# Kernel tuning notes

Hardware: AMD Instinct MI355X
Metric: run time of the kernel (lower is better)

## Reference

```python
import jax, jax.numpy as jnp
import numpy as np
from jax import lax

B, H0, W0 = 4, 64, 64
IN_DIM = 256; DIM = 256; HEADS = 8; WS = 8; HID = 1024
DH = DIM // HEADS          # 32, per-head dim
P = 16; K = 16             # DES decomposition: 256 = K * P


def hardswish(x):
    return x * jnp.clip(x + 3.0, 0.0, 6.0) * (1.0 / 6.0)


def layernorm(x, w, b):
    mu = jnp.mean(x, -1, keepdims=True)
    var = jnp.mean(jnp.square(x - mu), -1, keepdims=True)
    return (x - mu) * lax.rsqrt(var + 1e-5) * w + b


def dwconv(x, w, b, pad):
    # x: (B,C,H,W); w: (C,1,k,k) depthwise
    y = lax.conv_general_dilated(x, w, (1, 1), [(pad, pad), (pad, pad)],
                                 dimension_numbers=('NCHW', 'OIHW', 'NCHW'),
                                 feature_group_count=x.shape[1])
    return y + b[None, :, None, None]


def cross_attn(q, k, v, H, W, ws, d, scale, horizontal):
    # q,k,v: (B, N=H*W, C); C = h*d with h heads of dim d
    Bn, N, C = q.shape
    h = C // d
    if horizontal:
        G = H // ws
        def win(y):
            return y.reshape(Bn, G, ws, W, h, d).transpose(0, 1, 4, 2, 3, 5).reshape(Bn, G, h, ws * W, d)
    else:
        G = W // ws
        def win(y):
            return y.reshape(Bn, H, G, ws, h, d).transpose(0, 2, 4, 3, 1, 5).reshape(Bn, G, h, ws * H, d)
    qw, kw, vw = win(q), win(k), win(v)
    a = jax.nn.softmax(jnp.einsum('bghnd,bghmd->bghnm', qw, kw) * scale, axis=-1)
    o = jnp.einsum('bghnm,bghmd->bghnd', a, vw)
    if horizontal:
        o = o.reshape(Bn, G, h, ws, W, d).transpose(0, 1, 3, 4, 2, 5).reshape(Bn, H * W, C)
    else:
        o = o.reshape(Bn, G, h, ws, H, d).transpose(0, 4, 1, 3, 2, 5).reshape(Bn, H * W, C)
    return o


def setup_inputs() -> dict:
    key = jax.random.key(0)
    ks = jax.random.split(key, 12)
    r = lambda k, shape, s=0.02: jax.random.normal(k, shape, jnp.float32) * s
    return dict(
        x=jax.random.normal(ks[0], (B, H0 * W0, IN_DIM), jnp.float32),
        H=H0, W=W0,
        ln1_w=jnp.ones(IN_DIM, jnp.float32), ln1_b=jnp.zeros(IN_DIM, jnp.float32),
        Wqkv=r(ks[1], (IN_DIM, 2 * DIM)), bqkv=jnp.zeros(2 * DIM, jnp.float32),
        convp_w=r(ks[2], (DIM, 1, 3, 3), 0.1), convp_b=jnp.zeros(DIM, jnp.float32),
        Wout=r(ks[3], (DIM, DIM)), bout=jnp.zeros(DIM, jnp.float32),
        bn_g=jnp.ones(DIM, jnp.float32), bn_b=jnp.zeros(DIM, jnp.float32),
        des_wr=r(ks[4], (P, P), 0.1), des_br=jnp.zeros(P, jnp.float32),
        des_wl=r(ks[5], (K, K), 0.1), des_bl=jnp.zeros(K, jnp.float32),
        ln2_w=jnp.ones(IN_DIM, jnp.float32), ln2_b=jnp.zeros(IN_DIM, jnp.float32),
        fc1_w=r(ks[6], (IN_DIM, HID)), fc1_b=jnp.zeros(HID, jnp.float32),
        mix3_w=r(ks[7], (HID // 2, 1, 3, 3), 0.1), mix3_b=jnp.zeros(HID // 2, jnp.float32),
        mix5_w=r(ks[8], (HID // 2, 1, 5, 5), 0.1), mix5_b=jnp.zeros(HID // 2, jnp.float32),
        fc2_w=r(ks[9], (HID, DIM)), fc2_b=jnp.zeros(DIM, jnp.float32),
    )


def reference(x, H, W, ln1_w, ln1_b, Wqkv, bqkv, convp_w, convp_b, Wout, bout,
              bn_g, bn_b, des_wr, des_br, des_wl, des_bl, ln2_w, ln2_b,
              fc1_w, fc1_b, mix3_w, mix3_b, mix5_w, mix5_b, fc2_w, fc2_b):
    Bn, N, _ = x.shape
    res = x
    # ---- attention branch ----
    xn = layernorm(x, ln1_w, ln1_b)
    qv = xn @ Wqkv + bqkv                      # (B,N,2*DIM)
    q, v = jnp.split(qv, 2, axis=-1)
    # parallel depthwise conv on hardswish(v)
    v_img = hardswish(v.reshape(Bn, H, W, DIM).transpose(0, 3, 1, 2))
    v_conv = dwconv(v_img, convp_w, convp_b, 1).reshape(Bn, DIM, N).transpose(0, 2, 1)
    # cross-shaped window attention (k = v, per HRViT)
    qh, qvv = jnp.split(q, 2, axis=-1)
    vh, vv = jnp.split(v, 2, axis=-1)
    scale = DH ** -0.5
    ah = cross_attn(qh, vh, vh, H, W, WS, DH, scale, True)    # horizontal stripes
    av = cross_attn(qvv, vv, vv, H, W, WS, DH, scale, False)  # vertical stripes
    a = hardswish(jnp.concatenate([ah, av], axis=-1) + v_conv)
    a = a @ Wout + bout
    # BatchNorm1d over flattened (B*N, DIM), training-mode batch stats, eps=1e-5
    af = a.reshape(Bn * N, DIM)
    mu = jnp.mean(af, 0)
    var = jnp.mean(jnp.square(af - mu), 0)
    a = ((af - mu) * lax.rsqrt(var + 1e-5) * bn_g + bn_b).reshape(Bn, N, DIM)
    # DES shortcut on the residual
    xd = res.reshape(Bn, N, K, P) @ des_wr + des_br
    xd = jax.nn.gelu(xd.swapaxes(-1, -2), approximate=False)   # (B,N,P,K)
    xd = (xd @ des_wl + des_bl).swapaxes(-1, -2).reshape(Bn, N, DIM)
    x = a + xd + res
    # ---- MixCFN FFN branch ----
    res2 = x
    xn = layernorm(x, ln2_w, ln2_b)
    h1 = (xn @ fc1_w + fc1_b).transpose(0, 2, 1).reshape(Bn, HID, H, W)
    h1a, h1b = jnp.split(h1, 2, axis=1)
    hc = jnp.concatenate([dwconv(h1a, mix3_w, mix3_b, 1),
                          dwconv(h1b, mix5_w, mix5_b, 2)], axis=1)
    hc = jax.nn.gelu(hc, approximate=False).reshape(Bn, HID, N).transpose(0, 2, 1)
    return hc @ fc2_w + fc2_b + res2
```

## Files before the change

### kernel.cpp

```cpp
#include <hip/hip_runtime.h>
#include <hip/hip_bf16.h>

typedef __bf16 bf16;
typedef __bf16 bf16x8 __attribute__((ext_vector_type(8)));
typedef __bf16 bf16x4 __attribute__((ext_vector_type(4)));
typedef float f32x4 __attribute__((ext_vector_type(4)));

#define DEVFN static __device__ __forceinline__

DEVFN f32x4 mfma16(bf16x8 a, bf16x8 b, f32x4 c) {
  return __builtin_amdgcn_mfma_f32_16x16x32_bf16(a, b, c, 0, 0, 0);
}

DEVFN float hswish(float x) { return x * fminf(fmaxf(x + 3.f, 0.f), 6.f) * (1.f / 6.f); }
DEVFN float gelu_exact(float x) { return 0.5f * x * (1.f + erff(x * 0.70710678118654752f)); }

DEVFN unsigned packbf2(float lo, float hi) {
  union { bf16 h; unsigned short u; } a, b;
  a.h = (bf16)lo; b.h = (bf16)hi;
  return (unsigned)a.u | ((unsigned)b.u << 16);
}

DEVFN void async16(const void* g, void* l) {
  typedef __attribute__((address_space(3))) unsigned int lds_u32;
  typedef const __attribute__((address_space(1))) unsigned int glb_u32;
  __builtin_amdgcn_global_load_lds((glb_u32*)g, (lds_u32*)l, 16, 0, 0);
}

DEVFN int tmap(int dir, int b, int g, int m) {
  return dir == 0 ? (b * 4096 + g * 512 + m)
                  : (b * 4096 + (m & 63) * 64 + g * 8 + (m >> 6));
}

__global__ __launch_bounds__(256) void convert_x(const float* __restrict__ src,
                                                 bf16* __restrict__ dst) {
  long i = ((long)blockIdx.x * 256 + threadIdx.x) * 8;
  f32x4 a = *(const f32x4*)(src + i);
  f32x4 b = *(const f32x4*)(src + i + 4);
  bf16x8 o;
#pragma unroll
  for (int j = 0; j < 4; j++) { o[j] = (bf16)a[j]; o[4 + j] = (bf16)b[j]; }
  *(bf16x8*)(dst + i) = o;
}

struct ConvArgs { const float* s[24]; bf16* d[24]; };

__global__ __launch_bounds__(256) void convert_w(ConvArgs a) {
  static const int cum[25] = {0, 131072, 196608, 458752, 720896, 723200, 727808, 740608,
                              740864, 741120, 741632, 741888, 742144, 742400, 742656,
                              742912, 742928, 743184, 743200, 743456, 743712, 744736,
                              745248, 745760, 746016};
  static const int Kt[7] = {256, 256, 256, 1024, 256, 512, 512};
  static const int Nt[7] = {512, 256, 1024, 256, 9, 9, 25};
  int g = blockIdx.x * 256 + threadIdx.x;
  if (g >= 746016) return;
  int e = 0;
  while (g >= cum[e + 1]) e++;
  int i = g - cum[e];
  float v = a.s[e][i];
  int di = i;
  if (e < 7) di = (i % Nt[e]) * Kt[e] + i / Nt[e];
  a.d[e][di] = (bf16)v;
}

__global__ __launch_bounds__(256) void ln_kernel(const bf16* __restrict__ x,
                                                 const bf16* __restrict__ w,
                                                 const bf16* __restrict__ b,
                                                 bf16* __restrict__ out) {
  int tid = threadIdx.x, lane = tid & 63, wv = tid >> 6;
  long row = (long)blockIdx.x * 4 + wv;
  bf16x4 xv = *(const bf16x4*)(x + row * 256 + lane * 4);
  float v[4];
#pragma unroll
  for (int i = 0; i < 4; i++) v[i] = (float)xv[i];
  float s = v[0] + v[1] + v[2] + v[3];
#pragma unroll
  for (int m = 1; m < 64; m <<= 1) s += __shfl_xor(s, m);
  float mu = s * (1.f / 256.f);
  float q = 0.f;
#pragma unroll
  for (int i = 0; i < 4; i++) { float d = v[i] - mu; q += d * d; }
#pragma unroll
  for (int m = 1; m < 64; m <<= 1) q += __shfl_xor(q, m);
  float r = rsqrtf(q * (1.f / 256.f) + 1e-5f);
  bf16x4 wv4 = *(const bf16x4*)(w + lane * 4);
  bf16x4 bv4 = *(const bf16x4*)(b + lane * 4);
  bf16x4 o;
#pragma unroll
  for (int i = 0; i < 4; i++) o[i] = (bf16)((v[i] - mu) * r * (float)wv4[i] + (float)bv4[i]);
  *(bf16x4*)(out + row * 256 + lane * 4) = o;
}

__global__ __launch_bounds__(256) void gemm_bt(const bf16* __restrict__ A,
                                               const bf16* __restrict__ BT,
                                               const bf16* __restrict__ bias,
                                               const bf16* __restrict__ resid,
                                               bf16* __restrict__ C,
                                               float* __restrict__ Cf,
                                               int M, int N, int K) {
  __shared__ __align__(16) bf16 Asl[2][128 * 32];
  __shared__ __align__(16) bf16 Bsl[2][128 * 32];
  const int tid = threadIdx.x;
  const int lane = tid & 63, wid = tid >> 6;
  const int rowBase = blockIdx.x * 128, colBase = blockIdx.y * 128;
  f32x4 acc[4][4] = {};
  const int e0 = wid * 1024 + lane * 8;
  const int e1 = e0 + 512;
  const int r0 = e0 >> 5, c0 = e0 & 31;
  const int r1 = e1 >> 5, c1 = e1 & 31;
  const bf16* Ab0 = A + (long)(rowBase + r0) * K + c0;
  const bf16* Ab1 = A + (long)(rowBase + r1) * K + c1;
  const bf16* Bb0 = BT + (long)(colBase + r0) * K + c0;
  const bf16* Bb1 = BT + (long)(colBase + r1) * K + c1;
  const int wr = (wid >> 1) * 64, wc = (wid & 1) * 64;
  const int fr = lane & 15, fk = (lane >> 4) * 8;
  const int nIt = K >> 5;
  async16(Ab0, &Asl[0][wid * 1024]);
  async16(Ab1, &Asl[0][wid * 1024 + 512]);
  async16(Bb0, &Bsl[0][wid * 1024]);
  async16(Bb1, &Bsl[0][wid * 1024 + 512]);
  for (int it = 0; it < nIt; ++it) {
    const int cur = it & 1;
    __syncthreads();
    if (it + 1 < nIt) {
      const int nxt = cur ^ 1;
      const int k1 = (it + 1) << 5;
      async16(Ab0 + k1, &Asl[nxt][wid * 1024]);
      async16(Ab1 + k1, &Asl[nxt][wid * 1024 + 512]);
      async16(Bb0 + k1, &Bsl[nxt][wid * 1024]);
      async16(Bb1 + k1, &Bsl[nxt][wid * 1024 + 512]);
    }
    bf16x8 af[4], bfv[4];
#pragma unroll
    for (int m = 0; m < 4; m++) af[m] = *(const bf16x8*)&Asl[cur][(wr + m * 16 + fr) * 32 + fk];
#pragma unroll
    for (int n = 0; n < 4; n++) bfv[n] = *(const bf16x8*)&Bsl[cur][(wc + n * 16 + fr) * 32 + fk];
#pragma unroll
    for (int m = 0; m < 4; m++)
#pragma unroll
      for (int n = 0; n < 4; n++) acc[m][n] = mfma16(af[m], bfv[n], acc[m][n]);
  }
#pragma unroll
  for (int m = 0; m < 4; m++) {
#pragma unroll
    for (int r = 0; r < 4; r++) {
      int row = rowBase + wr + m * 16 + (lane >> 4) * 4 + r;
#pragma unroll
      for (int n = 0; n < 4; n++) {
        int col = colBase + wc + n * 16 + fr;
        float v = acc[m][n][r] + (float)bias[col];
        if (resid) v += (float)resid[(long)row * N + col];
        if (Cf) Cf[(long)row * N + col] = v;
        else C[(long)row * N + col] = (bf16)v;
      }
    }
  }
}

__global__ __launch_bounds__(256) void dwconv_v(const bf16* __restrict__ qv,
                                                const bf16* __restrict__ wt,
                                                const bf16* __restrict__ cb,
                                                bf16* __restrict__ vconv) {
  int bx = blockIdx.x;
  int wh = bx & 1, h = (bx >> 1) & 63, b = bx >> 7;
  int tid = threadIdx.x;
  int c0 = (tid & 31) * 8;
  int w0 = wh * 32 + (tid >> 5) * 4;
  long base = (long)b * 4096;
  float acc[4][8];
#pragma unroll
  for (int q = 0; q < 8; q++) {
    float bv = (float)cb[c0 + q];
#pragma unroll
    for (int i = 0; i < 4; i++) acc[i][q] = bv;
  }
#pragma unroll
  for (int ky = 0; ky < 3; ky++) {
    int hy = h + ky - 1;
    if ((unsigned)hy >= 64u) continue;
    float row[6][8];
#pragma unroll
    for (int j = 0; j < 6; j++) {
      int wx = w0 + j - 1;
      bool valid = (unsigned)wx < 64u;
      int wxc = valid ? wx : 0;
      bf16x8 iv = *(const bf16x8*)(qv + (base + hy * 64 + wxc) * 512 + 256 + c0);
#pragma unroll
      for (int q = 0; q < 8; q++) row[j][q] = valid ? hswish((float)iv[q]) : 0.f;
    }
#pragma unroll
    for (int kx = 0; kx < 3; kx++) {
      bf16x8 wv = *(const bf16x8*)(wt + (ky * 3 + kx) * 256 + c0);
      float wf[8];
#pragma unroll
      for (int q = 0; q < 8; q++) wf[q] = (float)wv[q];
#pragma unroll
      for (int i = 0; i < 4; i++)
#pragma unroll
        for (int q = 0; q < 8; q++) acc[i][q] += row[i + kx][q] * wf[q];
    }
  }
#pragma unroll
  for (int i = 0; i < 4; i++) {
    long t = base + h * 64 + w0 + i;
    bf16x8 o;
#pragma unroll
    for (int q = 0; q < 8; q++) o[q] = (bf16)acc[i][q];
    *(bf16x8*)(vconv + t * 256 + c0) = o;
  }
}

__global__ __launch_bounds__(256) void attn_kernel(const bf16* __restrict__ qv,
                                                   const bf16* __restrict__ vconv,
                                                   bf16* __restrict__ aout) {
  __shared__ __align__(16) bf16 Kl[512 * 32];
  __shared__ __align__(16) bf16 Vt[32 * 512];
  const int tid = threadIdx.x, lane = tid & 63, wid = tid >> 6;
  const int u = blockIdx.x >> 1, hf = blockIdx.x & 1;
  const int head = u & 3, g = (u >> 2) & 7, dir = (u >> 5) & 1, b = u >> 6;
  const int qch = dir * 128 + head * 32;
  const int vch = 256 + qch;
  char* KlB = (char*)Kl;
  char* VtB = (char*)Vt;

#pragma unroll
  for (int it = 0; it < 8; it++) {
    int task = it * 256 + tid;
    int t = task >> 2, cg = task & 3;
    long tk = tmap(dir, b, g, t);
    bf16x8 v = *(const bf16x8*)(qv + tk * 512 + vch + cg * 8);
    int byte = (t * 64 + cg * 16) ^ ((t & 7) << 4);
    *(bf16x8*)(KlB + byte) = v;
  }
  __syncthreads();
#pragma unroll
  for (int it = 0; it < 8; it++) {
    int task = it * 256 + tid;
    int ch = task & 31, kvb = task >> 5;
    int c = kvb >> 2, fb = kvb & 3;
    bf16 tv[8];
#pragma unroll
    for (int j = 0; j < 8; j++) {
      int kv = c * 32 + (j < 4 ? fb * 4 + j : 16 + fb * 4 + (j - 4));
      int byte = (kv * 64 + ch * 2) ^ ((kv & 7) << 4);
      tv[j] = *(const bf16*)(KlB + byte);
    }
    int wbyte = (ch * 1024 + kvb * 16) ^ ((ch & 7) << 4);
    *(bf16x8*)(VtB + wbyte) = *(bf16x8*)tv;
  }
  __syncthreads();

  const int fr = lane & 15, fkh = lane >> 4;
  const float scale = 0.17677669529663687f;
  const f32x4 zero = {0.f, 0.f, 0.f, 0.f};

  for (int qp = 0; qp < 2; ++qp) {
    int qrowA = hf * 256 + wid * 64 + qp * 32;
    int qrowB = qrowA + 16;
    long tqA = tmap(dir, b, g, qrowA + fr);
    long tqB = tmap(dir, b, g, qrowB + fr);
    bf16x8 qfA = *(const bf16x8*)(qv + tqA * 512 + qch + fkh * 8);
    bf16x8 qfB = *(const bf16x8*)(qv + tqB * 512 + qch + fkh * 8);
    float mA = 4.0f, lA = 0.f, mB = 4.0f, lB = 0.f;
    f32x4 oA0 = zero, oA1 = zero, oB0 = zero, oB1 = zero;
#pragma unroll
    for (int c = 0; c < 16; c++) {
      int kb0 = ((c * 32 + fr) * 64 + fkh * 16) ^ ((fr & 7) << 4);
      int kb1 = ((c * 32 + 16 + fr) * 64 + fkh * 16) ^ ((fr & 7) << 4);
      bf16x8 kf0 = *(const bf16x8*)(KlB + kb0);
      bf16x8 kf1 = *(const bf16x8*)(KlB + kb1);
      int vb = ((c * 32 + fkh * 8) * 2) ^ ((fr & 7) << 4);
      bf16x8 v0 = *(const bf16x8*)(VtB + fr * 1024 + vb);
      bf16x8 v1 = *(const bf16x8*)(VtB + (16 + fr) * 1024 + vb);
      f32x4 sA0 = mfma16(kf0, qfA, zero);
      f32x4 sA1 = mfma16(kf1, qfA, zero);
      f32x4 sB0 = mfma16(kf0, qfB, zero);
      f32x4 sB1 = mfma16(kf1, qfB, zero);
      float cmaxA = -1e30f, cmaxB = -1e30f;
#pragma unroll
      for (int r = 0; r < 4; r++) {
        sA0[r] *= scale; sA1[r] *= scale;
        sB0[r] *= scale; sB1[r] *= scale;
        cmaxA = fmaxf(cmaxA, fmaxf(sA0[r], sA1[r]));
        cmaxB = fmaxf(cmaxB, fmaxf(sB0[r], sB1[r]));
      }
      if (__any(cmaxA > mA + 8.f)) {
        float cm = cmaxA;
        cm = fmaxf(cm, __shfl_xor(cm, 16));
        cm = fmaxf(cm, __shfl_xor(cm, 32));
        float mn = fmaxf(mA, cm);
        float corr = __expf(mA - mn);
        lA *= corr;
        float c0c = __shfl(corr, fkh * 4 + 0);
        float c1c = __shfl(corr, fkh * 4 + 1);
        float c2c = __shfl(corr, fkh * 4 + 2);
        float c3c = __shfl(corr, fkh * 4 + 3);
        oA0[0] *= c0c; oA0[1] *= c1c; oA0[2] *= c2c; oA0[3] *= c3c;
        oA1[0] *= c0c; oA1[1] *= c1c; oA1[2] *= c2c; oA1[3] *= c3c;
        mA = mn;
      }
      if (__any(cmaxB > mB + 8.f)) {
        float cm = cmaxB;
        cm = fmaxf(cm, __shfl_xor(cm, 16));
        cm = fmaxf(cm, __shfl_xor(cm, 32));
        float mn = fmaxf(mB, cm);
        float corr = __expf(mB - mn);
        lB *= corr;
        float c0c = __shfl(corr, fkh * 4 + 0);
        float c1c = __shfl(corr, fkh * 4 + 1);
        float c2c = __shfl(corr, fkh * 4 + 2);
        float c3c = __shfl(corr, fkh * 4 + 3);
        oB0[0] *= c0c; oB0[1] *= c1c; oB0[2] *= c2c; oB0[3] *= c3c;
        oB1[0] *= c0c; oB1[1] *= c1c; oB1[2] *= c2c; oB1[3] *= c3c;
        mB = mn;
      }
      float pA0[4], pA1[4], pB0[4], pB1[4];
#pragma unroll
      for (int r = 0; r < 4; r++) {
        pA0[r] = __expf(sA0[r] - mA);
        pA1[r] = __expf(sA1[r] - mA);
        pB0[r] = __expf(sB0[r] - mB);
        pB1[r] = __expf(sB1[r] - mB);
        lA += pA0[r] + pA1[r];
        lB += pB0[r] + pB1[r];
      }
      union { unsigned u[4]; bf16x8 v8; } paA, paB;
      paA.u[0] = packbf2(pA0[0], pA0[1]);
      paA.u[1] = packbf2(pA0[2], pA0[3]);
      paA.u[2] = packbf2(pA1[0], pA1[1]);
      paA.u[3] = packbf2(pA1[2], pA1[3]);
      paB.u[0] = packbf2(pB0[0], pB0[1]);
      paB.u[1] = packbf2(pB0[2], pB0[3]);
      paB.u[2] = packbf2(pB1[0], pB1[1]);
      paB.u[3] = packbf2(pB1[2], pB1[3]);
      oA0 = mfma16(paA.v8, v0, oA0);
      oA1 = mfma16(paA.v8, v1, oA1);
      oB0 = mfma16(paB.v8, v0, oB0);
      oB1 = mfma16(paB.v8, v1, oB1);
    }
    float ltA = lA;
    ltA += __shfl_xor(ltA, 16);
    ltA += __shfl_xor(ltA, 32);
    float invA = 1.f / ltA;
    float ltB = lB;
    ltB += __shfl_xor(ltB, 16);
    ltB += __shfl_xor(ltB, 32);
    float invB = 1.f / ltB;
    float iA[4], iB[4];
#pragma unroll
    for (int r = 0; r < 4; r++) {
      iA[r] = __shfl(invA, fkh * 4 + r);
      iB[r] = __shfl(invB, fkh * 4 + r);
    }
#pragma unroll
    for (int r = 0; r < 4; r++) {
      int rowA = qrowA + fkh * 4 + r;
      long toA = tmap(dir, b, g, rowA);
      float vc0 = (float)vconv[toA * 256 + qch + fr];
      float vc1 = (float)vconv[toA * 256 + qch + 16 + fr];
      aout[toA * 256 + qch + fr] = (bf16)hswish(oA0[r] * iA[r] + vc0);
      aout[toA * 256 + qch + 16 + fr] = (bf16)hswish(oA1[r] * iA[r] + vc1);
      int rowB = qrowB + fkh * 4 + r;
      long toB = tmap(dir, b, g, rowB);
      float wc0 = (float)vconv[toB * 256 + qch + fr];
      float wc1 = (float)vconv[toB * 256 + qch + 16 + fr];
      aout[toB * 256 + qch + fr] = (bf16)hswish(oB0[r] * iB[r] + wc0);
      aout[toB * 256 + qch + 16 + fr] = (bf16)hswish(oB1[r] * iB[r] + wc1);
    }
  }
}

__global__ __launch_bounds__(256) void bn_part(const bf16* __restrict__ a2,
                                               float* __restrict__ part) {
  int tid = threadIdx.x, bx = blockIdx.x;
  int c0 = (tid & 31) * 8, rg = tid >> 5;
  float s[8] = {}, q[8] = {};
  for (int i = 0; i < 32; i++) {
    long row = (long)bx * 256 + rg * 32 + i;
    bf16x8 v = *(const bf16x8*)(a2 + row * 256 + c0);
#pragma unroll
    for (int j = 0; j < 8; j++) { float f = (float)v[j]; s[j] += f; q[j] += f * f; }
  }
  long pb = (long)bx * 8 + rg;
#pragma unroll
  for (int j = 0; j < 8; j++) {
    part[pb * 256 + c0 + j] = s[j];
    part[131072 + pb * 256 + c0 + j] = q[j];
  }
}

__global__ void bn_final(const float* __restrict__ part, const bf16* __restrict__ g,
                         const bf16* __restrict__ bb, float* __restrict__ coef) {
  int c = threadIdx.x;
  float s = 0.f, q = 0.f;
  for (int i = 0; i < 512; i++) { s += part[i * 256 + c]; q += part[131072 + i * 256 + c]; }
  float mu = s * (1.f / 16384.f);
  float var = q * (1.f / 16384.f) - mu * mu;
  float sc = (float)g[c] * rsqrtf(var + 1e-5f);
  coef[c] = sc;
  coef[256 + c] = (float)bb[c] - mu * sc;
}

__global__ __launch_bounds__(256) void des_combine(const bf16* __restrict__ x,
                                                   const bf16* __restrict__ a2,
                                                   const float* __restrict__ coef,
                                                   const bf16* __restrict__ wr,
                                                   const bf16* __restrict__ br,
                                                   const bf16* __restrict__ wl,
                                                   const bf16* __restrict__ bl,
                                                   bf16* __restrict__ x2) {
  __shared__ float X[4][256], M1[4][256];
  __shared__ float WR[256], WL[256], BR[16], BL[16], SC[256], SH[256];
  int tid = threadIdx.x, lane = tid & 63, wvi = tid >> 6;
  WR[tid] = (float)wr[tid];
  WL[tid] = (float)wl[tid];
  SC[tid] = coef[tid];
  SH[tid] = coef[256 + tid];
  if (tid < 16) { BR[tid] = (float)br[tid]; BL[tid] = (float)bl[tid]; }
  long t = (long)blockIdx.x * 4 + wvi;
  bf16x4 xv = *(const bf16x4*)(x + t * 256 + lane * 4);
#pragma unroll
  for (int i = 0; i < 4; i++) X[wvi][lane * 4 + i] = (float)xv[i];
  __syncthreads();
#pragma unroll
  for (int u2 = 0; u2 < 4; u2++) {
    int e = u2 * 64 + lane, k = e >> 4, p = e & 15;
    float acc = BR[p];
#pragma unroll
    for (int p2 = 0; p2 < 16; p2++) acc += X[wvi][k * 16 + p2] * WR[p2 * 16 + p];
    M1[wvi][e] = gelu_exact(acc);
  }
  __syncthreads();
#pragma unroll
  for (int u2 = 0; u2 < 4; u2++) {
    int e = u2 * 64 + lane, k = e >> 4, p = e & 15;
    float acc = BL[k];
#pragma unroll
    for (int k2 = 0; k2 < 16; k2++) acc += M1[wvi][k2 * 16 + p] * WL[k2 * 16 + k];
    float a2v = (float)a2[t * 256 + e];
    x2[t * 256 + e] = (bf16)(SC[e] * a2v + SH[e] + acc + X[wvi][e]);
  }
}

__global__ __launch_bounds__(256) void mixconv(const bf16* __restrict__ h1,
                                               const bf16* __restrict__ wt3,
                                               const bf16* __restrict__ b3,
                                               const bf16* __restrict__ wt5,
                                               const bf16* __restrict__ b5,
                                               bf16* __restrict__ hc) {
  int bx = blockIdx.x;
  int slice = bx & 3, wh = (bx >> 2) & 1, h = (bx >> 3) & 63, b = bx >> 9;
  int tid = threadIdx.x;
  int c0 = slice * 256 + (tid & 31) * 8;
  int w0 = wh * 32 + (tid >> 5) * 4;
  bool five = slice >= 2;
  int cc = five ? c0 - 512 : c0;
  long base = (long)b * 4096;
  float acc[4][8];
  {
    const bf16* bp = (five ? b5 : b3) + cc;
#pragma unroll
    for (int q = 0; q < 8; q++) {
      float bv = (float)bp[q];
#pragma unroll
      for (int i = 0; i < 4; i++) acc[i][q] = bv;
    }
  }
  if (!five) {
    const bf16* wbase = wt3 + cc;
#pragma unroll
    for (int ky = 0; ky < 3; ky++) {
      int hy = h + ky - 1;
      if ((unsigned)hy >= 64u) continue;
      float row[6][8];
#pragma unroll
      for (int j = 0; j < 6; j++) {
        int wx = w0 + j - 1;
        bool valid = (unsigned)wx < 64u;
        int wxc = valid ? wx : 0;
        bf16x8 iv = *(const bf16x8*)(h1 + (base + hy * 64 + wxc) * 1024 + c0);
#pragma unroll
        for (int q = 0; q < 8; q++) row[j][q] = valid ? (float)iv[q] : 0.f;
      }
#pragma unroll
      for (int kx = 0; kx < 3; kx++) {
        bf16x8 wv = *(const bf16x8*)(wbase + (ky * 3 + kx) * 512);
        float wf[8];
#pragma unroll
        for (int q = 0; q < 8; q++) wf[q] = (float)wv[q];
#pragma unroll
        for (int i = 0; i < 4; i++)
#pragma unroll
          for (int q = 0; q < 8; q++) acc[i][q] += row[i + kx][q] * wf[q];
      }
    }
  } else {
    const bf16* wbase = wt5 + cc;
#pragma unroll
    for (int ky = 0; ky < 5; ky++) {
      int hy = h + ky - 2;
      if ((unsigned)hy >= 64u) continue;
      float row[8][8];
#pragma unroll
      for (int j = 0; j < 8; j++) {
        int wx = w0 + j - 2;
        bool valid = (unsigned)wx < 64u;
        int wxc = valid ? wx : 0;
        bf16x8 iv = *(const bf16x8*)(h1 + (base + hy * 64 + wxc) * 1024 + c0);
#pragma unroll
        for (int q = 0; q < 8; q++) row[j][q] = valid ? (float)iv[q] : 0.f;
      }
#pragma unroll
      for (int kx = 0; kx < 5; kx++) {
        bf16x8 wv = *(const bf16x8*)(wbase + (ky * 5 + kx) * 512);
        float wf[8];
#pragma unroll
        for (int q = 0; q < 8; q++) wf[q] = (float)wv[q];
#pragma unroll
        for (int i = 0; i < 4; i++)
#pragma unroll
          for (int q = 0; q < 8; q++) acc[i][q] += row[i + kx][q] * wf[q];
      }
    }
  }
#pragma unroll
  for (int i = 0; i < 4; i++) {
    long t = base + h * 64 + w0 + i;
    bf16x8 o;
#pragma unroll
    for (int q = 0; q < 8; q++) o[q] = (bf16)gelu_exact(acc[i][q]);
    *(bf16x8*)(hc + t * 1024 + c0) = o;
  }
}

extern "C" void kernel_launch(void* const* d_in, const int* in_sizes, int n_in,
                              void* d_out, int out_size, void* d_ws, size_t ws_size,
                              hipStream_t stream) {
  if (ws_size < 92274688ull) return;

  char* ws = (char*)d_ws;
  float* bncoef = (float*)(ws + 256);
  char* Dc = ws + 4096;
  auto alloc = [&](size_t bytes) { bf16* p = (bf16*)Dc; Dc += (bytes + 255) & ~(size_t)255; return p; };
  bf16* cx      = alloc(8388608);
  bf16* cWqkvT  = alloc(262144);
  bf16* cWoutT  = alloc(131072);
  bf16* cfc1T   = alloc(524288);
  bf16* cfc2T   = alloc(524288);
  bf16* cconvp  = alloc(4608);
  bf16* cwt3    = alloc(9216);
  bf16* cwt5    = alloc(25600);
  bf16* cln1w   = alloc(512);
  bf16* cln1b   = alloc(512);
  bf16* cbqkv   = alloc(1024);
  bf16* cconvpb = alloc(512);
  bf16* cbout   = alloc(512);
  bf16* cbng    = alloc(512);
  bf16* cbnb    = alloc(512);
  bf16* cdwr    = alloc(512);
  bf16* cdbr    = alloc(32);
  bf16* cdwl    = alloc(512);
  bf16* cdbl    = alloc(32);
  bf16* cln2w   = alloc(512);
  bf16* cln2b   = alloc(512);
  bf16* cfc1b   = alloc(2048);
  bf16* cm3b    = alloc(1024);
  bf16* cm5b    = alloc(1024);
  bf16* cfc2b   = alloc(512);
  bf16* qv    = (bf16*)(ws + 16777216);
  bf16* vconv = (bf16*)(ws + 33554432);
  bf16* attn  = (bf16*)(ws + 41943040);
  bf16* h1    = (bf16*)(ws + 16777216);
  bf16* xnb     = (bf16*)(ws + 50331648);
  bf16* a2      = (bf16*)(ws + 58720256);
  float* bnpart = (float*)(ws + 67108864);
  bf16* hc      = (bf16*)(ws + 50331648);
  bf16* x2 = (bf16*)(ws + 83886080);

  convert_x<<<2048, 256, 0, stream>>>((const float*)d_in[0], cx);
  ConvArgs ca;
  const int srcIdx[24] = {5, 9, 19, 25, 7, 21, 23, 3, 4, 6, 8, 10, 11, 12,
                          13, 14, 15, 16, 17, 18, 20, 22, 24, 26};
  bf16* dsts[24] = {cWqkvT, cWoutT, cfc1T, cfc2T, cconvp, cwt3, cwt5, cln1w, cln1b,
                    cbqkv, cconvpb, cbout, cbng, cbnb, cdwr, cdbr, cdwl, cdbl,
                    cln2w, cln2b, cfc1b, cm3b, cm5b, cfc2b};
  for (int i = 0; i < 24; i++) { ca.s[i] = (const float*)d_in[srcIdx[i]]; ca.d[i] = dsts[i]; }
  convert_w<<<2916, 256, 0, stream>>>(ca);

  ln_kernel<<<4096, 256, 0, stream>>>(cx, cln1w, cln1b, xnb);
  gemm_bt<<<dim3(128, 4), 256, 0, stream>>>(xnb, cWqkvT, cbqkv, nullptr, qv, nullptr, 16384, 512, 256);
  dwconv_v<<<512, 256, 0, stream>>>(qv, cconvp, cconvpb, vconv);
  attn_kernel<<<512, 256, 0, stream>>>(qv, vconv, attn);
  gemm_bt<<<dim3(128, 2), 256, 0, stream>>>(attn, cWoutT, cbout, nullptr, a2, nullptr, 16384, 256, 256);
  bn_part<<<64, 256, 0, stream>>>(a2, bnpart);
  bn_final<<<1, 256, 0, stream>>>(bnpart, cbng, cbnb, bncoef);
  des_combine<<<4096, 256, 0, stream>>>(cx, a2, bncoef, cdwr, cdbr, cdwl, cdbl, x2);
  ln_kernel<<<4096, 256, 0, stream>>>(x2, cln2w, cln2b, xnb);
  gemm_bt<<<dim3(128, 8), 256, 0, stream>>>(xnb, cfc1T, cfc1b, nullptr, h1, nullptr, 16384, 1024, 256);
  mixconv<<<2048, 256, 0, stream>>>(h1, cwt3, cm3b, cwt5, cm5b, hc);
  gemm_bt<<<dim3(128, 2), 256, 0, stream>>>(hc, cfc2T, cfc2b, x2, nullptr, (float*)d_out, 16384, 256, 1024);
}
```

Measured before the change: 253.5 us.

## Fuse input conversion with LN1, BN stats into GEMM, LN2 into DES combine

Merges the fp32-to-bf16 input conversion with the first layernorm, computes BatchNorm partial sums and sums of squares in the output-projection GEMM epilogue instead of a separate pass, and folds the second layernorm into the DES combine kernel. This drops three launches and several full passes over 16384x256 activations. BN partials are now computed from fp32 values before bf16 rounding, a slight numerical difference, and the GEMM epilogue gains shuffles and extra stores.

```diff
diff --git a/kernel.cpp b/kernel.cpp
--- a/kernel.cpp
+++ b/kernel.cpp
@@ -32,15 +32,34 @@
                   : (b * 4096 + (m & 63) * 64 + g * 8 + (m >> 6));
 }
 
-__global__ __launch_bounds__(256) void convert_x(const float* __restrict__ src,
-                                                 bf16* __restrict__ dst) {
-  long i = ((long)blockIdx.x * 256 + threadIdx.x) * 8;
-  f32x4 a = *(const f32x4*)(src + i);
-  f32x4 b = *(const f32x4*)(src + i + 4);
-  bf16x8 o;
-#pragma unroll
-  for (int j = 0; j < 4; j++) { o[j] = (bf16)a[j]; o[4 + j] = (bf16)b[j]; }
-  *(bf16x8*)(dst + i) = o;
+__global__ __launch_bounds__(256) void convx_ln(const float* __restrict__ src,
+                                                const bf16* __restrict__ w,
+                                                const bf16* __restrict__ b,
+                                                bf16* __restrict__ cx,
+                                                bf16* __restrict__ xnb) {
+  int tid = threadIdx.x, lane = tid & 63, wv = tid >> 6;
+  long row = (long)blockIdx.x * 4 + wv;
+  f32x4 xv = *(const f32x4*)(src + row * 256 + lane * 4);
+  bf16x4 cxo;
+#pragma unroll
+  for (int i = 0; i < 4; i++) cxo[i] = (bf16)xv[i];
+  *(bf16x4*)(cx + row * 256 + lane * 4) = cxo;
+  float s = xv[0] + xv[1] + xv[2] + xv[3];
+#pragma unroll
+  for (int m = 1; m < 64; m <<= 1) s += __shfl_xor(s, m);
+  float mu = s * (1.f / 256.f);
+  float q = 0.f;
+#pragma unroll
+  for (int i = 0; i < 4; i++) { float d = xv[i] - mu; q += d * d; }
+#pragma unroll
+  for (int m = 1; m < 64; m <<= 1) q += __shfl_xor(q, m);
+  float r = rsqrtf(q * (1.f / 256.f) + 1e-5f);
+  bf16x4 wv4 = *(const bf16x4*)(w + lane * 4);
+  bf16x4 bv4 = *(const bf16x4*)(b + lane * 4);
+  bf16x4 o;
+#pragma unroll
+  for (int i = 0; i < 4; i++) o[i] = (bf16)((xv[i] - mu) * r * (float)wv4[i] + (float)bv4[i]);
+  *(bf16x4*)(xnb + row * 256 + lane * 4) = o;
 }
 
 struct ConvArgs { const float* s[24]; bf16* d[24]; };
@@ -63,40 +82,13 @@
   a.d[e][di] = (bf16)v;
 }
 
-__global__ __launch_bounds__(256) void ln_kernel(const bf16* __restrict__ x,
-                                                 const bf16* __restrict__ w,
-                                                 const bf16* __restrict__ b,
-                                                 bf16* __restrict__ out) {
-  int tid = threadIdx.x, lane = tid & 63, wv = tid >> 6;
-  long row = (long)blockIdx.x * 4 + wv;
-  bf16x4 xv = *(const bf16x4*)(x + row * 256 + lane * 4);
-  float v[4];
-#pragma unroll
-  for (int i = 0; i < 4; i++) v[i] = (float)xv[i];
-  float s = v[0] + v[1] + v[2] + v[3];
-#pragma unroll
-  for (int m = 1; m < 64; m <<= 1) s += __shfl_xor(s, m);
-  float mu = s * (1.f / 256.f);
-  float q = 0.f;
-#pragma unroll
-  for (int i = 0; i < 4; i++) { float d = v[i] - mu; q += d * d; }
-#pragma unroll
-  for (int m = 1; m < 64; m <<= 1) q += __shfl_xor(q, m);
-  float r = rsqrtf(q * (1.f / 256.f) + 1e-5f);
-  bf16x4 wv4 = *(const bf16x4*)(w + lane * 4);
-  bf16x4 bv4 = *(const bf16x4*)(b + lane * 4);
-  bf16x4 o;
-#pragma unroll
-  for (int i = 0; i < 4; i++) o[i] = (bf16)((v[i] - mu) * r * (float)wv4[i] + (float)bv4[i]);
-  *(bf16x4*)(out + row * 256 + lane * 4) = o;
-}
-
 __global__ __launch_bounds__(256) void gemm_bt(const bf16* __restrict__ A,
                                                const bf16* __restrict__ BT,
                                                const bf16* __restrict__ bias,
                                                const bf16* __restrict__ resid,
                                                bf16* __restrict__ C,
                                                float* __restrict__ Cf,
+                                               float* __restrict__ bnp,
                                                int M, int N, int K) {
   __shared__ __align__(16) bf16 Asl[2][128 * 32];
   __shared__ __align__(16) bf16 Bsl[2][128 * 32];
@@ -140,6 +132,7 @@
 #pragma unroll
       for (int n = 0; n < 4; n++) acc[m][n] = mfma16(af[m], bfv[n], acc[m][n]);
   }
+  float cs[4] = {}, cq[4] = {};
 #pragma unroll
   for (int m = 0; m < 4; m++) {
 #pragma unroll
@@ -150,8 +143,23 @@
         int col = colBase + wc + n * 16 + fr;
         float v = acc[m][n][r] + (float)bias[col];
         if (resid) v += (float)resid[(long)row * N + col];
+        if (bnp) { cs[n] += v; cq[n] += v * v; }
         if (Cf) Cf[(long)row * N + col] = v;
         else C[(long)row * N + col] = (bf16)v;
+      }
+    }
+  }
+  if (bnp) {
+#pragma unroll
+    for (int n = 0; n < 4; n++) {
+      float s = cs[n], q = cq[n];
+      s += __shfl_xor(s, 16); s += __shfl_xor(s, 32);
+      q += __shfl_xor(q, 16); q += __shfl_xor(q, 32);
+      if ((lane >> 4) == 0) {
+        int slot = blockIdx.x * 2 + (wid >> 1);
+        int gcol = colBase + wc + n * 16 + fr;
+        bnp[slot * 256 + gcol] = s;
+        bnp[65536 + slot * 256 + gcol] = q;
       }
     }
   }
@@ -370,30 +378,11 @@
   }
 }
 
-__global__ __launch_bounds__(256) void bn_part(const bf16* __restrict__ a2,
-                                               float* __restrict__ part) {
-  int tid = threadIdx.x, bx = blockIdx.x;
-  int c0 = (tid & 31) * 8, rg = tid >> 5;
-  float s[8] = {}, q[8] = {};
-  for (int i = 0; i < 32; i++) {
-    long row = (long)bx * 256 + rg * 32 + i;
-    bf16x8 v = *(const bf16x8*)(a2 + row * 256 + c0);
-#pragma unroll
-    for (int j = 0; j < 8; j++) { float f = (float)v[j]; s[j] += f; q[j] += f * f; }
-  }
-  long pb = (long)bx * 8 + rg;
-#pragma unroll
-  for (int j = 0; j < 8; j++) {
-    part[pb * 256 + c0 + j] = s[j];
-    part[131072 + pb * 256 + c0 + j] = q[j];
-  }
-}
-
 __global__ void bn_final(const float* __restrict__ part, const bf16* __restrict__ g,
                          const bf16* __restrict__ bb, float* __restrict__ coef) {
   int c = threadIdx.x;
   float s = 0.f, q = 0.f;
-  for (int i = 0; i < 512; i++) { s += part[i * 256 + c]; q += part[131072 + i * 256 + c]; }
+  for (int i = 0; i < 256; i++) { s += part[i * 256 + c]; q += part[65536 + i * 256 + c]; }
   float mu = s * (1.f / 16384.f);
   float var = q * (1.f / 16384.f) - mu * mu;
   float sc = (float)g[c] * rsqrtf(var + 1e-5f);
@@ -401,21 +390,26 @@
   coef[256 + c] = (float)bb[c] - mu * sc;
 }
 
-__global__ __launch_bounds__(256) void des_combine(const bf16* __restrict__ x,
-                                                   const bf16* __restrict__ a2,
-                                                   const float* __restrict__ coef,
-                                                   const bf16* __restrict__ wr,
-                                                   const bf16* __restrict__ br,
-                                                   const bf16* __restrict__ wl,
-                                                   const bf16* __restrict__ bl,
-                                                   bf16* __restrict__ x2) {
+__global__ __launch_bounds__(256) void des_combine_ln(const bf16* __restrict__ x,
+                                                      const bf16* __restrict__ a2,
+                                                      const float* __restrict__ coef,
+                                                      const bf16* __restrict__ wr,
+                                                      const bf16* __restrict__ br,
+                                                      const bf16* __restrict__ wl,
+                                                      const bf16* __restrict__ bl,
+                                                      const bf16* __restrict__ ln2w,
+                                                      const bf16* __restrict__ ln2b,
+                                                      bf16* __restrict__ x2,
+                                                      bf16* __restrict__ xnb) {
   __shared__ float X[4][256], M1[4][256];
-  __shared__ float WR[256], WL[256], BR[16], BL[16], SC[256], SH[256];
+  __shared__ float WR[256], WL[256], BR[16], BL[16], SC[256], SH[256], W2[256], B2[256];
   int tid = threadIdx.x, lane = tid & 63, wvi = tid >> 6;
   WR[tid] = (float)wr[tid];
   WL[tid] = (float)wl[tid];
   SC[tid] = coef[tid];
   SH[tid] = coef[256 + tid];
+  W2[tid] = (float)ln2w[tid];
+  B2[tid] = (float)ln2b[tid];
   if (tid < 16) { BR[tid] = (float)br[tid]; BL[tid] = (float)bl[tid]; }
   long t = (long)blockIdx.x * 4 + wvi;
   bf16x4 xv = *(const bf16x4*)(x + t * 256 + lane * 4);
@@ -431,6 +425,7 @@
     M1[wvi][e] = gelu_exact(acc);
   }
   __syncthreads();
+  float v4[4];
 #pragma unroll
   for (int u2 = 0; u2 < 4; u2++) {
     int e = u2 * 64 + lane, k = e >> 4, p = e & 15;
@@ -438,7 +433,23 @@
 #pragma unroll
     for (int k2 = 0; k2 < 16; k2++) acc += M1[wvi][k2 * 16 + p] * WL[k2 * 16 + k];
     float a2v = (float)a2[t * 256 + e];
-    x2[t * 256 + e] = (bf16)(SC[e] * a2v + SH[e] + acc + X[wvi][e]);
+    v4[u2] = SC[e] * a2v + SH[e] + acc + X[wvi][e];
+  }
+  float s = v4[0] + v4[1] + v4[2] + v4[3];
+#pragma unroll
+  for (int m = 1; m < 64; m <<= 1) s += __shfl_xor(s, m);
+  float mu = s * (1.f / 256.f);
+  float q = 0.f;
+#pragma unroll
+  for (int i = 0; i < 4; i++) { float d = v4[i] - mu; q += d * d; }
+#pragma unroll
+  for (int m = 1; m < 64; m <<= 1) q += __shfl_xor(q, m);
+  float r = rsqrtf(q * (1.f / 256.f) + 1e-5f);
+#pragma unroll
+  for (int u2 = 0; u2 < 4; u2++) {
+    int e = u2 * 64 + lane;
+    x2[t * 256 + e] = (bf16)v4[u2];
+    xnb[t * 256 + e] = (bf16)((v4[u2] - mu) * r * W2[e] + B2[e]);
   }
 }
 
@@ -577,7 +588,6 @@
   bf16* hc      = (bf16*)(ws + 50331648);
   bf16* x2 = (bf16*)(ws + 83886080);
 
-  convert_x<<<2048, 256, 0, stream>>>((const float*)d_in[0], cx);
   ConvArgs ca;
   const int srcIdx[24] = {5, 9, 19, 25, 7, 21, 23, 3, 4, 6, 8, 10, 11, 12,
                           13, 14, 15, 16, 17, 18, 20, 22, 24, 26};
@@ -586,17 +596,16 @@
                     cln2w, cln2b, cfc1b, cm3b, cm5b, cfc2b};
   for (int i = 0; i < 24; i++) { ca.s[i] = (const float*)d_in[srcIdx[i]]; ca.d[i] = dsts[i]; }
   convert_w<<<2916, 256, 0, stream>>>(ca);
-
-  ln_kernel<<<4096, 256, 0, stream>>>(cx, cln1w, cln1b, xnb);
-  gemm_bt<<<dim3(128, 4), 256, 0, stream>>>(xnb, cWqkvT, cbqkv, nullptr, qv, nullptr, 16384, 512, 256);
+  convx_ln<<<4096, 256, 0, stream>>>((const float*)d_in[0], cln1w, cln1b, cx, xnb);
+
+  gemm_bt<<<dim3(128, 4), 256, 0, stream>>>(xnb, cWqkvT, cbqkv, nullptr, qv, nullptr, nullptr, 16384, 512, 256);
   dwconv_v<<<512, 256, 0, stream>>>(qv, cconvp, cconvpb, vconv);
   attn_kernel<<<512, 256, 0, stream>>>(qv, vconv, attn);
-  gemm_bt<<<dim3(128, 2), 256, 0, stream>>>(attn, cWoutT, cbout, nullptr, a2, nullptr, 16384, 256, 256);
-  bn_part<<<64, 256, 0, stream>>>(a2, bnpart);
+  gemm_bt<<<dim3(128, 2), 256, 0, stream>>>(attn, cWoutT, cbout, nullptr, a2, nullptr, bnpart, 16384, 256, 256);
   bn_final<<<1, 256, 0, stream>>>(bnpart, cbng, cbnb, bncoef);
-  des_combine<<<4096, 256, 0, stream>>>(cx, a2, bncoef, cdwr, cdbr, cdwl, cdbl, x2);
-  ln_kernel<<<4096, 256, 0, stream>>>(x2, cln2w, cln2b, xnb);
-  gemm_bt<<<dim3(128, 8), 256, 0, stream>>>(xnb, cfc1T, cfc1b, nullptr, h1, nullptr, 16384, 1024, 256);
+  des_combine_ln<<<4096, 256, 0, stream>>>(cx, a2, bncoef, cdwr, cdbr, cdwl, cdbl,
+                                           cln2w, cln2b, x2, xnb);
+  gemm_bt<<<dim3(128, 8), 256, 0, stream>>>(xnb, cfc1T, cfc1b, nullptr, h1, nullptr, nullptr, 16384, 1024, 256);
   mixconv<<<2048, 256, 0, stream>>>(h1, cwt3, cm3b, cwt5, cm5b, hc);
-  gemm_bt<<<dim3(128, 2), 256, 0, stream>>>(hc, cfc2T, cfc2b, x2, nullptr, (float*)d_out, 16384, 256, 1024);
-}
+  gemm_bt<<<dim3(128, 2), 256, 0, stream>>>(hc, cfc2T, cfc2b, x2, nullptr, (float*)d_out, nullptr, 16384, 256, 1024);
+}
```

Measured after the change: 229.9 us. 9.3% less time.
